# Kernel optimization log

Hardware: AMD Instinct MI355X
Metric: run time of the kernel (lower is better)

## Reference

```python
import jax, jax.numpy as jnp
import numpy as np

EMBED_DIM = 1024
NUM_HEADS = 16
HEAD_DIM = EMBED_DIM // NUM_HEADS
NEG = -1000000000.0


def setup_inputs() -> dict:
    key = jax.random.key(0)
    ks = jax.random.split(key, 13)
    B, S, D = 4, 2048, EMBED_DIM
    scale = 1.0 / np.sqrt(D)
    inp = {
        "query": jax.random.normal(ks[0], (B, S, D), jnp.float32),
        "key": jax.random.normal(ks[1], (B, S, D), jnp.float32),
        "value": jax.random.normal(ks[2], (B, S, D), jnp.float32),
        "mask": jax.random.randint(ks[3], (B, 1, 1, S), 0, 2, jnp.int32),
        "Wq": jax.random.normal(ks[4], (D, D), jnp.float32) * scale,
        "bq": jnp.zeros((D,), jnp.float32),
        "Wk": jax.random.normal(ks[5], (D, D), jnp.float32) * scale,
        "bk": jnp.zeros((D,), jnp.float32),
        "Wv": jax.random.normal(ks[6], (D, D), jnp.float32) * scale,
        "bv": jnp.zeros((D,), jnp.float32),
        "Wo": jax.random.normal(ks[7], (D, D), jnp.float32) * scale,
        "bo": jnp.zeros((D,), jnp.float32),
    }
    return inp


def _split_heads(x):
    B, S, D = x.shape
    return x.reshape(B, S, NUM_HEADS, HEAD_DIM).transpose(0, 2, 1, 3)  # [B,H,S,hd]


def reference(query, key, value, mask, Wq, bq, Wk, bk, Wv, bv, Wo, bo):
    B, S, D = query.shape
    Q = _split_heads(query @ Wq + bq)
    K = _split_heads(key @ Wk + bk)
    V = _split_heads(value @ Wv + bv)
    scores = jnp.einsum("bhqd,bhkd->bhqk", Q, K) / jnp.sqrt(jnp.float32(HEAD_DIM))
    scores = jnp.where(mask == 0, jnp.float32(NEG), scores)
    attn = jax.nn.softmax(scores, axis=-1)
    out = jnp.einsum("bhqk,bhkd->bhqd", attn, V)
    out = out.transpose(0, 2, 1, 3).reshape(B, S, D)
    return out @ Wo + bo
```

## Files before the change

kernel.cpp:

```cpp
#include <hip/hip_runtime.h>


#define SEQ   2048
#define EDIM  1024
#define NHEAD 16
#define HDIM  64
#define NBAT  4
#define MTOK  8192

typedef __attribute__((ext_vector_type(8))) __bf16 bf16x8;
typedef __attribute__((ext_vector_type(4))) __bf16 bf16x4;
typedef __attribute__((ext_vector_type(4))) float f32x4;
typedef __attribute__((ext_vector_type(16))) float f32x16;
typedef __attribute__((ext_vector_type(8))) unsigned short us8;
typedef unsigned short u16;

#define SCL   0.1803368801111244f

__device__ __forceinline__ u16 bfbits(float f) {
    __bf16 h = (__bf16)f;
    return __builtin_bit_cast(u16, h);
}
__device__ __forceinline__ bf16x8 bc(us8 v) { return __builtin_bit_cast(bf16x8, v); }
__device__ __forceinline__ float exp2fast(float x) {
    float r;
    asm("v_exp_f32 %0, %1" : "=v"(r) : "v"(x));
    return r;
}
__device__ __forceinline__ void glds16(const void* g, void* l) {
    __builtin_amdgcn_global_load_lds(
        (const __attribute__((address_space(1))) unsigned int*)g,
        (__attribute__((address_space(3))) unsigned int*)l, 16, 0, 0);
}

__global__ __launch_bounds__(256) void prep_kernel(const int* __restrict__ mask,
                                                   int* __restrict__ idxl,
                                                   int* __restrict__ cntp) {
    __shared__ int psum[257];
    const int b = blockIdx.x, t = threadIdx.x;
    const int* mp = mask + b * SEQ;
    int m8[8]; int s = 0;
#pragma unroll
    for (int i = 0; i < 8; ++i) { m8[i] = mp[t * 8 + i]; s += (m8[i] != 0); }
    psum[t + 1] = s;
    __syncthreads();
    if (t == 0) { psum[0] = 0; for (int i = 1; i <= 256; ++i) psum[i] += psum[i - 1]; }
    __syncthreads();
    int ex = psum[t];
#pragma unroll
    for (int i = 0; i < 8; ++i)
        if (m8[i] != 0) idxl[b * SEQ + (ex++)] = t * 8 + i;
    if (t == 0) cntp[b] = psum[256];
}

__global__ __launch_bounds__(256) void wtrans4_kernel(const float* __restrict__ W0,
                                                      const float* __restrict__ W1,
                                                      const float* __restrict__ W2,
                                                      const float* __restrict__ W3,
                                                      u16* __restrict__ WT) {
    __shared__ float tile[32][33];
    const int tx = threadIdx.x, ty = threadIdx.y;
    const int bx = blockIdx.x,  by = blockIdx.y, wz = blockIdx.z;
    const float* W = (wz == 0) ? W0 : (wz == 1) ? W1 : (wz == 2) ? W2 : W3;
    u16* O = WT + (size_t)wz * EDIM * EDIM;
#pragma unroll
    for (int i = 0; i < 4; ++i)
        tile[ty + i * 8][tx] = W[(size_t)(by * 32 + ty + i * 8) * EDIM + bx * 32 + tx];
    __syncthreads();
#pragma unroll
    for (int i = 0; i < 4; ++i) {
        int n = bx * 32 + ty + i * 8;
        int k = by * 32 + tx;
        O[(size_t)n * EDIM + k] = bfbits(tile[tx][ty + i * 8]);
    }
}

__global__ __launch_bounds__(256) void qkv_gemm_kernel(
        const float* __restrict__ Aq, const float* __restrict__ Ak,
        const float* __restrict__ Av, const u16* __restrict__ WTall,
        const float* __restrict__ bqp, const float* __restrict__ bkp,
        const float* __restrict__ bvp,
        u16* __restrict__ Qb, u16* __restrict__ Kb, u16* __restrict__ Vb,
        const int* __restrict__ idxl, const int* __restrict__ cntp) {
    const int id    = blockIdx.x;
    const int which = id >> 9;
    const int sub   = id & 511;
    const int r_    = sub >> 3;
    const int grp   = r_ >> 5, bnq = (r_ >> 2) & 7, bmin = r_ & 3;
    const int bm    = (sub & 7) + 8 * (grp * 4 + bmin);
    const int bn    = bnq;

    const float* A    = (which == 0) ? Aq : (which == 1) ? Ak : Av;
    const u16*   WT   = WTall + (size_t)which * EDIM * EDIM;
    const float* bias = (which == 0) ? bqp : (which == 1) ? bkp : bvp;
    u16*         outp = (which == 0) ? Qb : (which == 1) ? Kb : Vb;
    const float  oscale = (which == 1) ? SCL : 1.0f;
    const bool   gather = (which > 0);

    int cn = SEQ;
    if (gather) {
        cn = cntp[bm >> 4];
        if (((bm & 15) * 128) >= cn) return;
    }

    __shared__ __align__(16) float As[2][128 * 32];
    __shared__ __align__(16) u16   Bs[2][128][32];

    const int tid  = threadIdx.x;
    const int lane = tid & 63, w = tid >> 6;
    const int g    = lane >> 4, l15 = lane & 15;
    const int wrow = w >> 1, wcol = w & 1;

    const char* pa[4];
#pragma unroll
    for (int t = 0; t < 4; ++t) {
        const int rloc = w * 32 + t * 8 + (lane >> 3);
        int arow;
        if (gather) {
            const int sloc = (bm & 15) * 128 + rloc;
            const int gi = (sloc < cn) ? idxl[(bm >> 4) * SEQ + sloc] : 0;
            arow = (bm >> 4) * SEQ + gi;
        } else arow = bm * 128 + rloc;
        const int scol = ((lane & 7) ^ (lane >> 3)) * 4;
        pa[t] = (const char*)(A + (size_t)arow * EDIM + scol);
    }
    const char* pb[2];
#pragma unroll
    for (int t = 0; t < 2; ++t) {
        const int rloc = w * 32 + t * 16 + (lane >> 2);
        const int brow = bn * 128 + rloc;
        const int scol = ((lane & 3) ^ ((lane >> 3) & 3)) * 8;
        pb[t] = (const char*)(WT + (size_t)brow * EDIM + scol);
    }

    auto STAGE = [&](int bufn, int ko) {
        char* abase = (char*)&As[bufn][0] + w * 4096;
#pragma unroll
        for (int t = 0; t < 4; ++t)
            glds16(pa[t] + (size_t)ko * 4, abase + t * 1024);
        char* bbase = (char*)&Bs[bufn][0][0] + w * 2048;
#pragma unroll
        for (int t = 0; t < 2; ++t)
            glds16(pb[t] + (size_t)ko * 2, bbase + t * 1024);
    };

    f32x4 acc[4][4] = {};
    constexpr int NT = EDIM / 32;

    STAGE(0, 0);
    __syncthreads();

    int buf = 0;
#pragma unroll 1
    for (int kt = 0; kt < NT; ++kt) {
        if (kt < NT - 1) STAGE(buf ^ 1, (kt + 1) * 32);

        bf16x8 af[4], bfr[4];
        {
            const float* Ab = &As[buf][0];
            const int x = l15 & 7;
#pragma unroll
            for (int i = 0; i < 4; ++i) {
                const int row = wrow * 64 + i * 16 + l15;
                f32x4 u0 = *(const f32x4*)(Ab + row * 32 + (((2 * g)     ^ x) * 4));
                f32x4 u1 = *(const f32x4*)(Ab + row * 32 + (((2 * g + 1) ^ x) * 4));
#pragma unroll
                for (int j = 0; j < 4; ++j) {
                    af[i][j]     = (__bf16)u0[j];
                    af[i][4 + j] = (__bf16)u1[j];
                }
            }
        }
        {
            const int x = (l15 >> 1) & 3;
#pragma unroll
            for (int j = 0; j < 4; ++j) {
                const int row = wcol * 64 + j * 16 + l15;
                bfr[j] = bc(*(const us8*)((const u16*)&Bs[buf][0][0] + row * 32 + ((g ^ x) * 8)));
            }
        }

#pragma unroll
        for (int i = 0; i < 4; ++i)
#pragma unroll
            for (int j = 0; j < 4; ++j)
                acc[i][j] = __builtin_amdgcn_mfma_f32_16x16x32_bf16(af[i], bfr[j], acc[i][j], 0, 0, 0);

        __syncthreads();
        buf ^= 1;
    }

#pragma unroll
    for (int i = 0; i < 4; ++i) {
#pragma unroll
        for (int j = 0; j < 4; ++j) {
            const int gm0 = bm * 128 + wrow * 64 + i * 16 + g * 4;
            const int gn  = bn * 128 + wcol * 64 + j * 16 + l15;
            const float bv = bias[gn];
#pragma unroll
            for (int r = 0; r < 4; ++r) {
                float val = (acc[i][j][r] + bv) * oscale;
                const int m = gm0 + r;
                if (gather && (m & 2047) >= cn) val = 0.f;
                const int b = m >> 11, s = m & 2047;
                const int h = gn >> 6, d = gn & 63;
                if (which == 2)
                    outp[((size_t)(b * NHEAD + h) << 17) + d * SEQ + s] = bfbits(val);
                else
                    outp[((size_t)(b * NHEAD + h) << 17) + s * HDIM + d] = bfbits(val);
            }
        }
    }
}

__global__ __launch_bounds__(256) void o_gemm_kernel(const u16* __restrict__ Ap,
                                                     const u16* __restrict__ WT,
                                                     const float* __restrict__ bias,
                                                     float* __restrict__ outp) {
    const int id  = blockIdx.x;
    const int r_  = id >> 3;
    const int grp = r_ >> 5, bnq = (r_ >> 2) & 7, bmin = r_ & 3;
    const int bm  = (id & 7) + 8 * (grp * 4 + bmin);
    const int bn  = bnq;

    __shared__ __align__(16) u16 As[2][128][32];
    __shared__ __align__(16) u16 Bs[2][128][32];

    const int tid  = threadIdx.x;
    const int lane = tid & 63, w = tid >> 6;
    const int g    = lane >> 4, l15 = lane & 15;
    const int wrow = w >> 1, wcol = w & 1;

    const char* pa[2]; const char* pb[2];
#pragma unroll
    for (int t = 0; t < 2; ++t) {
        const int rloc = w * 32 + t * 16 + (lane >> 2);
        const int scol = ((lane & 3) ^ ((lane >> 3) & 3)) * 8;
        pa[t] = (const char*)(Ap + (size_t)(bm * 128 + rloc) * EDIM + scol);
        pb[t] = (const char*)(WT + (size_t)(bn * 128 + rloc) * EDIM + scol);
    }

    auto STAGE = [&](int bufn, int ko) {
        char* abase = (char*)&As[bufn][0][0] + w * 2048;
        char* bbase = (char*)&Bs[bufn][0][0] + w * 2048;
#pragma unroll
        for (int t = 0; t < 2; ++t) {
            glds16(pa[t] + (size_t)ko * 2, abase + t * 1024);
            glds16(pb[t] + (size_t)ko * 2, bbase + t * 1024);
        }
    };

    f32x4 acc[4][4] = {};
    constexpr int NT = EDIM / 32;

    STAGE(0, 0);
    __syncthreads();

    int buf = 0;
#pragma unroll 1
    for (int kt = 0; kt < NT; ++kt) {
        if (kt < NT - 1) STAGE(buf ^ 1, (kt + 1) * 32);

        bf16x8 af[4], bfr[4];
        const int x = (l15 >> 1) & 3;
#pragma unroll
        for (int i = 0; i < 4; ++i) {
            const int rowA = wrow * 64 + i * 16 + l15;
            af[i] = bc(*(const us8*)((const u16*)&As[buf][0][0] + rowA * 32 + ((g ^ x) * 8)));
            const int rowB = wcol * 64 + i * 16 + l15;
            bfr[i] = bc(*(const us8*)((const u16*)&Bs[buf][0][0] + rowB * 32 + ((g ^ x) * 8)));
        }

#pragma unroll
        for (int i = 0; i < 4; ++i)
#pragma unroll
            for (int j = 0; j < 4; ++j)
                acc[i][j] = __builtin_amdgcn_mfma_f32_16x16x32_bf16(af[i], bfr[j], acc[i][j], 0, 0, 0);

        __syncthreads();
        buf ^= 1;
    }

#pragma unroll
    for (int i = 0; i < 4; ++i) {
#pragma unroll
        for (int j = 0; j < 4; ++j) {
            const int gm0 = bm * 128 + wrow * 64 + i * 16 + g * 4;
            const int gn  = bn * 128 + wcol * 64 + j * 16 + l15;
            const float bv = bias[gn];
#pragma unroll
            for (int r = 0; r < 4; ++r)
                outp[(size_t)(gm0 + r) * EDIM + gn] = acc[i][j][r] + bv;
        }
    }
}

__global__ __launch_bounds__(256) void attn_kernel(const u16* __restrict__ Q,
                                                   const u16* __restrict__ K,
                                                   const u16* __restrict__ VT,
                                                   const int* __restrict__ cntp,
                                                   u16* __restrict__ O) {
    __shared__ u16 Klds[2][64][64];
    __shared__ u16 Vlds[2][64][64];

    const int tid = threadIdx.x, lane = tid & 63, w = tid >> 6;
    const int h = lane >> 5, l31 = lane & 31;

    const int id  = blockIdx.x;
    const int bh  = (id & 7) * 8 + ((id >> 3) >> 4);
    const int qb  = (id >> 3) & 15;
    const int b   = bh >> 4, hd_ = bh & 15;

    const u16* Qp = Q + ((size_t)bh << 17);
    const u16* Kp = K + ((size_t)bh << 17);
    const u16* Vp = VT + ((size_t)bh << 17);
    const int q0w = qb * 128 + w * 32;

    const int cn  = cntp[b];
    const int ktc = (cn + 63) >> 6;

    bf16x8 qf[4];
#pragma unroll
    for (int khd = 0; khd < 4; ++khd)
        qf[khd] = bc(*(const us8*)&Qp[(size_t)(q0w + l31) * HDIM + khd * 16 + h * 8]);

    const int b_  = l31 & 3, hp = (l31 >> 2) & 1, cc = l31 >> 3;
    const int piR = 16 * (cc & 1) + 8 * hp + 4 * (cc >> 1) + b_;
    const int swk = b_ | (hp << 2);
    const int swv = l31 & 7;

    const int lr = lane >> 3, lg = lane & 7;
    const u16* pKs[2]; const u16* pVs[2];
#pragma unroll
    for (int t = 0; t < 2; ++t) {
        const int rloc = w * 16 + t * 8 + lr;
        const int xk = (rloc & 3) | (((rloc >> 3) & 1) << 2);
        pKs[t] = Kp + (size_t)rloc * HDIM + ((lg ^ xk) << 3);
        const int xv = rloc & 7;
        pVs[t] = Vp + (size_t)rloc * SEQ + ((lg ^ xv) << 3);
    }

    auto STAGE = [&](int bufn, int kb) {
#pragma unroll
        for (int t = 0; t < 2; ++t) {
            glds16(pKs[t] + (size_t)kb * HDIM, &Klds[bufn][w * 16 + t * 8][0]);
            glds16(pVs[t] + kb,                &Vlds[bufn][w * 16 + t * 8][0]);
        }
    };

    f32x16 ot[2] = {};
    f32x16 ls = {};

    bf16x8 onesf;
#pragma unroll
    for (int j = 0; j < 8; ++j) onesf[j] = (__bf16)1.0f;

    STAGE(0, 0);
    __syncthreads();

    for (int kt = 0; kt < ktc; ++kt) {
        const int cur = kt & 1;
        const bool more = (kt + 1) < ktc;
        if (more) STAGE(cur ^ 1, (kt + 1) * 64);

        f32x16 st[2] = {};
        __builtin_amdgcn_s_setprio(1);
#pragma unroll
        for (int kb2 = 0; kb2 < 2; ++kb2) {
            const u16* Kr = &Klds[cur][kb2 * 32 + piR][0];
#pragma unroll
            for (int khd = 0; khd < 4; ++khd) {
                bf16x8 kf = bc(*(const us8*)&Kr[(khd * 16 + h * 8) ^ (swk << 3)]);
                st[kb2] = __builtin_amdgcn_mfma_f32_32x32x16_bf16(kf, qf[khd], st[kb2], 0, 0, 0);
            }
        }
        __builtin_amdgcn_s_setprio(0);

#pragma unroll
        for (int kb2 = 0; kb2 < 2; ++kb2)
#pragma unroll
            for (int e = 0; e < 16; ++e)
                st[kb2][e] = exp2fast(st[kb2][e]);

        if (kt == ktc - 1) {
            const int kbase = kt * 64;
#pragma unroll
            for (int kb2 = 0; kb2 < 2; ++kb2)
#pragma unroll
                for (int cp = 0; cp < 4; ++cp)
#pragma unroll
                    for (int j = 0; j < 4; ++j) {
                        const int key = kbase + kb2 * 32 + 16 * (cp & 1) + 4 * (cp >> 1) + 8 * h + j;
                        if (key >= cn) st[kb2][cp * 4 + j] = 0.f;
                    }
        }

        bf16x8 pf[4];
#pragma unroll
        for (int s = 0; s < 4; ++s) {
            const int kb2 = s >> 1, sel = (s & 1) * 4;
#pragma unroll
            for (int j = 0; j < 4; ++j) {
                pf[s][j]     = (__bf16)st[kb2][sel + j];
                pf[s][4 + j] = (__bf16)st[kb2][8 + sel + j];
            }
        }

        __builtin_amdgcn_s_setprio(1);
#pragma unroll
        for (int s = 0; s < 4; ++s)
            ls = __builtin_amdgcn_mfma_f32_32x32x16_bf16(onesf, pf[s], ls, 0, 0, 0);
#pragma unroll
        for (int dblk = 0; dblk < 2; ++dblk) {
            const u16* Vr = &Vlds[cur][dblk * 32 + l31][0];
#pragma unroll
            for (int s = 0; s < 4; ++s) {
                bf16x8 vf = bc(*(const us8*)&Vr[(s * 16 + h * 8) ^ (swv << 3)]);
                ot[dblk] = __builtin_amdgcn_mfma_f32_32x32x16_bf16(vf, pf[s], ot[dblk], 0, 0, 0);
            }
        }
        __builtin_amdgcn_s_setprio(0);

        __syncthreads();
    }

    const float inv = 1.f / ls[0];

    const size_t row = (size_t)(b * SEQ + q0w + l31) * EDIM + hd_ * HDIM;
#pragma unroll
    for (int dblk = 0; dblk < 2; ++dblk) {
#pragma unroll
        for (int cp = 0; cp < 4; ++cp) {
            bf16x4 t;
#pragma unroll
            for (int j = 0; j < 4; ++j)
                t[j] = (__bf16)(ot[dblk][cp * 4 + j] * inv);
            *(bf16x4*)&O[row + dblk * 32 + 8 * cp + 4 * h] = t;
        }
    }
}

extern "C" void kernel_launch(void* const* d_in, const int* in_sizes, int n_in,
                              void* d_out, int out_size, void* d_ws, size_t ws_size,
                              hipStream_t stream) {
    const float* query = (const float*)d_in[0];
    const float* key   = (const float*)d_in[1];
    const float* value = (const float*)d_in[2];
    const int*   mask  = (const int*)d_in[3];
    const float* Wq = (const float*)d_in[4];  const float* bq = (const float*)d_in[5];
    const float* Wk = (const float*)d_in[6];  const float* bk = (const float*)d_in[7];
    const float* Wv = (const float*)d_in[8];  const float* bv = (const float*)d_in[9];
    const float* Wo = (const float*)d_in[10]; const float* bo = (const float*)d_in[11];

    char* ws = (char*)d_ws;
    const size_t WT_BYTES  = (size_t)EDIM * EDIM * 2;
    const size_t BUF_BYTES = (size_t)MTOK * EDIM * 2;
    u16* wtq   = (u16*)(ws);
    u16* wto   = (u16*)(ws + 3 * WT_BYTES);
    u16* Qbuf  = (u16*)(ws + 4 * WT_BYTES);
    u16* Kbuf  = (u16*)(ws + 4 * WT_BYTES + BUF_BYTES);
    u16* VTbuf = (u16*)(ws + 4 * WT_BYTES + 2 * BUF_BYTES);
    u16* Abuf  = (u16*)(ws + 4 * WT_BYTES + 3 * BUF_BYTES);
    int* idxl  = (int*)(ws + 4 * WT_BYTES + 4 * BUF_BYTES);
    int* cntp  = (int*)(ws + 4 * WT_BYTES + 4 * BUF_BYTES + (size_t)MTOK * 4);

    prep_kernel<<<NBAT, 256, 0, stream>>>(mask, idxl, cntp);

    dim3 tgrid(32, 32, 4), tblk(32, 8);
    wtrans4_kernel<<<tgrid, tblk, 0, stream>>>(Wq, Wk, Wv, Wo, wtq);

    qkv_gemm_kernel<<<1536, 256, 0, stream>>>(query, key, value, wtq,
                                              bq, bk, bv, Qbuf, Kbuf, VTbuf,
                                              idxl, cntp);

    attn_kernel<<<1024, 256, 0, stream>>>(Qbuf, Kbuf, VTbuf, cntp, Abuf);

    o_gemm_kernel<<<512, 256, 0, stream>>>(Abuf, wto, bo, (float*)d_out);
}
```

Baseline: 179.7 us.

## Convert A tile to bf16 in registers before LDS store in QKV GEMM

The fp32 activation tile for the QKV projection GEMM is now loaded into registers, converted to bf16 once, and written to LDS as bf16, replacing async global-to-LDS copies of fp32 data. Each element is now converted once per block rather than once per consuming wave, and the A tile takes half the LDS space and read bandwidth. The price is that the A global load is no longer a direct LDS copy: its latency must be hidden by the MFMA work between the register load and the deferred LDS write, and register pressure goes up.

```diff
diff --git a/kernel.cpp b/kernel.cpp
--- a/kernel.cpp
+++ b/kernel.cpp
@@ -103,27 +103,30 @@
         if (((bm & 15) * 128) >= cn) return;
     }
 
-    __shared__ __align__(16) float As[2][128 * 32];
-    __shared__ __align__(16) u16   Bs[2][128][32];
+    __shared__ __align__(16) u16 As[2][128][32];
+    __shared__ __align__(16) u16 Bs[2][128][32];
 
     const int tid  = threadIdx.x;
     const int lane = tid & 63, w = tid >> 6;
     const int g    = lane >> 4, l15 = lane & 15;
     const int wrow = w >> 1, wcol = w & 1;
 
-    const char* pa[4];
-#pragma unroll
-    for (int t = 0; t < 4; ++t) {
-        const int rloc = w * 32 + t * 8 + (lane >> 3);
+    const float* paf[2];
+    int rlocA[2];
+#pragma unroll
+    for (int t = 0; t < 2; ++t) {
+        const int rloc = w * 32 + t * 16 + (lane >> 2);
+        rlocA[t] = rloc;
         int arow;
         if (gather) {
             const int sloc = (bm & 15) * 128 + rloc;
             const int gi = (sloc < cn) ? idxl[(bm >> 4) * SEQ + sloc] : 0;
             arow = (bm >> 4) * SEQ + gi;
         } else arow = bm * 128 + rloc;
-        const int scol = ((lane & 7) ^ (lane >> 3)) * 4;
-        pa[t] = (const char*)(A + (size_t)arow * EDIM + scol);
-    }
+        paf[t] = A + (size_t)arow * EDIM + (lane & 3) * 8;
+    }
+    const int xA = ((lane & 3) ^ ((lane >> 3) & 3)) * 8;
+
     const char* pb[2];
 #pragma unroll
     for (int t = 0; t < 2; ++t) {
@@ -133,11 +136,27 @@
         pb[t] = (const char*)(WT + (size_t)brow * EDIM + scol);
     }
 
-    auto STAGE = [&](int bufn, int ko) {
-        char* abase = (char*)&As[bufn][0] + w * 4096;
-#pragma unroll
-        for (int t = 0; t < 4; ++t)
-            glds16(pa[t] + (size_t)ko * 4, abase + t * 1024);
+    f32x4 ar[2][2];
+    auto LOAD_A = [&](int ko) {
+#pragma unroll
+        for (int t = 0; t < 2; ++t) {
+            ar[t][0] = *(const f32x4*)(paf[t] + ko);
+            ar[t][1] = *(const f32x4*)(paf[t] + ko + 4);
+        }
+    };
+    auto WRITE_A = [&](int bufn) {
+#pragma unroll
+        for (int t = 0; t < 2; ++t) {
+            bf16x8 o;
+#pragma unroll
+            for (int j = 0; j < 4; ++j) {
+                o[j]     = (__bf16)ar[t][0][j];
+                o[4 + j] = (__bf16)ar[t][1][j];
+            }
+            *(bf16x8*)&As[bufn][rlocA[t]][xA] = o;
+        }
+    };
+    auto STAGE_B = [&](int bufn, int ko) {
         char* bbase = (char*)&Bs[bufn][0][0] + w * 2048;
 #pragma unroll
         for (int t = 0; t < 2; ++t)
@@ -147,37 +166,28 @@
     f32x4 acc[4][4] = {};
     constexpr int NT = EDIM / 32;
 
-    STAGE(0, 0);
+    LOAD_A(0);
+    STAGE_B(0, 0);
+    WRITE_A(0);
     __syncthreads();
 
     int buf = 0;
 #pragma unroll 1
     for (int kt = 0; kt < NT; ++kt) {
-        if (kt < NT - 1) STAGE(buf ^ 1, (kt + 1) * 32);
+        const bool more = kt + 1 < NT;
+        if (more) {
+            LOAD_A((kt + 1) * 32);
+            STAGE_B(buf ^ 1, (kt + 1) * 32);
+        }
 
         bf16x8 af[4], bfr[4];
-        {
-            const float* Ab = &As[buf][0];
-            const int x = l15 & 7;
-#pragma unroll
-            for (int i = 0; i < 4; ++i) {
-                const int row = wrow * 64 + i * 16 + l15;
-                f32x4 u0 = *(const f32x4*)(Ab + row * 32 + (((2 * g)     ^ x) * 4));
-                f32x4 u1 = *(const f32x4*)(Ab + row * 32 + (((2 * g + 1) ^ x) * 4));
-#pragma unroll
-                for (int j = 0; j < 4; ++j) {
-                    af[i][j]     = (__bf16)u0[j];
-                    af[i][4 + j] = (__bf16)u1[j];
-                }
-            }
-        }
-        {
-            const int x = (l15 >> 1) & 3;
-#pragma unroll
-            for (int j = 0; j < 4; ++j) {
-                const int row = wcol * 64 + j * 16 + l15;
-                bfr[j] = bc(*(const us8*)((const u16*)&Bs[buf][0][0] + row * 32 + ((g ^ x) * 8)));
-            }
+        const int x = (l15 >> 1) & 3;
+#pragma unroll
+        for (int i = 0; i < 4; ++i) {
+            const int rowA = wrow * 64 + i * 16 + l15;
+            af[i] = bc(*(const us8*)((const u16*)&As[buf][0][0] + rowA * 32 + ((g ^ x) * 8)));
+            const int rowB = wcol * 64 + i * 16 + l15;
+            bfr[i] = bc(*(const us8*)((const u16*)&Bs[buf][0][0] + rowB * 32 + ((g ^ x) * 8)));
         }
 
 #pragma unroll
@@ -186,6 +196,7 @@
             for (int j = 0; j < 4; ++j)
                 acc[i][j] = __builtin_amdgcn_mfma_f32_16x16x32_bf16(af[i], bfr[j], acc[i][j], 0, 0, 0);
 
+        if (more) WRITE_A(buf ^ 1);
         __syncthreads();
         buf ^= 1;
     }
```

After: 192.1 us. 6.9% more time.

## Pre-convert and gather Q/K/V inputs to bf16 before the QKV GEMM

Applied to the files above, without the earlier changes.

Adds a separate kernel that casts the fp32 query/key/value activations to bf16 and compacts the unmasked key/value rows into contiguous buffers, zero-padding up to the next 128-row tile. The QKV GEMM then streams bf16 A tiles with the same swizzled LDS layout as the weights, which halves its A-side LDS footprint and global traffic and drops the per-fragment fp32-to-bf16 conversion and row-index gather. In exchange, an extra pass reads all fp32 inputs once and writes bf16 copies, and the new buffers share workspace with the attention output buffer.

```diff
diff --git a/kernel.cpp b/kernel.cpp
--- a/kernel.cpp
+++ b/kernel.cpp
@@ -75,13 +75,59 @@
     }
 }
 
+__global__ __launch_bounds__(256) void cvtg_kernel(const float* __restrict__ q,
+                                                   const float* __restrict__ k,
+                                                   const float* __restrict__ v,
+                                                   const int* __restrict__ idxl,
+                                                   const int* __restrict__ cntp,
+                                                   u16* __restrict__ oq,
+                                                   u16* __restrict__ ok,
+                                                   u16* __restrict__ ov) {
+    const int sel  = blockIdx.y;
+    const int grow = blockIdx.x * 4 + (threadIdx.x >> 6);
+    const int col  = (threadIdx.x & 63) * 16;
+    const float* src;
+    u16* dst;
+    if (sel == 0) {
+        src = q + (size_t)grow * EDIM;
+        dst = oq + (size_t)grow * EDIM;
+    } else {
+        const int b = grow >> 11, j = grow & 2047;
+        const int cn = cntp[b];
+        dst = (sel == 1 ? ok : ov) + (size_t)grow * EDIM;
+        if (j < cn) {
+            const int gi = idxl[b * SEQ + j];
+            src = (sel == 1 ? k : v) + ((size_t)(b * SEQ + gi)) * EDIM;
+        } else {
+            if (j < ((cn + 127) & ~127)) {
+                us8 z = {};
+                *(us8*)(dst + col) = z;
+                *(us8*)(dst + col + 8) = z;
+            }
+            return;
+        }
+    }
+    f32x4 v0 = *(const f32x4*)(src + col);
+    f32x4 v1 = *(const f32x4*)(src + col + 4);
+    f32x4 v2 = *(const f32x4*)(src + col + 8);
+    f32x4 v3 = *(const f32x4*)(src + col + 12);
+    us8 r0, r1;
+#pragma unroll
+    for (int j2 = 0; j2 < 4; ++j2) {
+        r0[j2] = bfbits(v0[j2]); r0[4 + j2] = bfbits(v1[j2]);
+        r1[j2] = bfbits(v2[j2]); r1[4 + j2] = bfbits(v3[j2]);
+    }
+    *(us8*)(dst + col) = r0;
+    *(us8*)(dst + col + 8) = r1;
+}
+
 __global__ __launch_bounds__(256) void qkv_gemm_kernel(
-        const float* __restrict__ Aq, const float* __restrict__ Ak,
-        const float* __restrict__ Av, const u16* __restrict__ WTall,
+        const u16* __restrict__ Aq, const u16* __restrict__ Ak,
+        const u16* __restrict__ Av, const u16* __restrict__ WTall,
         const float* __restrict__ bqp, const float* __restrict__ bkp,
         const float* __restrict__ bvp,
         u16* __restrict__ Qb, u16* __restrict__ Kb, u16* __restrict__ Vb,
-        const int* __restrict__ idxl, const int* __restrict__ cntp) {
+        const int* __restrict__ cntp) {
     const int id    = blockIdx.x;
     const int which = id >> 9;
     const int sub   = id & 511;
@@ -90,58 +136,43 @@
     const int bm    = (sub & 7) + 8 * (grp * 4 + bmin);
     const int bn    = bnq;
 
-    const float* A    = (which == 0) ? Aq : (which == 1) ? Ak : Av;
+    const u16*   A    = (which == 0) ? Aq : (which == 1) ? Ak : Av;
     const u16*   WT   = WTall + (size_t)which * EDIM * EDIM;
     const float* bias = (which == 0) ? bqp : (which == 1) ? bkp : bvp;
     u16*         outp = (which == 0) ? Qb : (which == 1) ? Kb : Vb;
     const float  oscale = (which == 1) ? SCL : 1.0f;
-    const bool   gather = (which > 0);
 
     int cn = SEQ;
-    if (gather) {
+    if (which > 0) {
         cn = cntp[bm >> 4];
         if (((bm & 15) * 128) >= cn) return;
     }
 
-    __shared__ __align__(16) float As[2][128 * 32];
-    __shared__ __align__(16) u16   Bs[2][128][32];
+    __shared__ __align__(16) u16 As[2][128][32];
+    __shared__ __align__(16) u16 Bs[2][128][32];
 
     const int tid  = threadIdx.x;
     const int lane = tid & 63, w = tid >> 6;
     const int g    = lane >> 4, l15 = lane & 15;
     const int wrow = w >> 1, wcol = w & 1;
 
-    const char* pa[4];
-#pragma unroll
-    for (int t = 0; t < 4; ++t) {
-        const int rloc = w * 32 + t * 8 + (lane >> 3);
-        int arow;
-        if (gather) {
-            const int sloc = (bm & 15) * 128 + rloc;
-            const int gi = (sloc < cn) ? idxl[(bm >> 4) * SEQ + sloc] : 0;
-            arow = (bm >> 4) * SEQ + gi;
-        } else arow = bm * 128 + rloc;
-        const int scol = ((lane & 7) ^ (lane >> 3)) * 4;
-        pa[t] = (const char*)(A + (size_t)arow * EDIM + scol);
-    }
-    const char* pb[2];
+    const char* pa[2]; const char* pb[2];
 #pragma unroll
     for (int t = 0; t < 2; ++t) {
         const int rloc = w * 32 + t * 16 + (lane >> 2);
-        const int brow = bn * 128 + rloc;
         const int scol = ((lane & 3) ^ ((lane >> 3) & 3)) * 8;
-        pb[t] = (const char*)(WT + (size_t)brow * EDIM + scol);
+        pa[t] = (const char*)(A + (size_t)(bm * 128 + rloc) * EDIM + scol);
+        pb[t] = (const char*)(WT + (size_t)(bn * 128 + rloc) * EDIM + scol);
     }
 
     auto STAGE = [&](int bufn, int ko) {
-        char* abase = (char*)&As[bufn][0] + w * 4096;
-#pragma unroll
-        for (int t = 0; t < 4; ++t)
-            glds16(pa[t] + (size_t)ko * 4, abase + t * 1024);
+        char* abase = (char*)&As[bufn][0][0] + w * 2048;
         char* bbase = (char*)&Bs[bufn][0][0] + w * 2048;
 #pragma unroll
-        for (int t = 0; t < 2; ++t)
+        for (int t = 0; t < 2; ++t) {
+            glds16(pa[t] + (size_t)ko * 2, abase + t * 1024);
             glds16(pb[t] + (size_t)ko * 2, bbase + t * 1024);
+        }
     };
 
     f32x4 acc[4][4] = {};
@@ -156,28 +187,13 @@
         if (kt < NT - 1) STAGE(buf ^ 1, (kt + 1) * 32);
 
         bf16x8 af[4], bfr[4];
-        {
-            const float* Ab = &As[buf][0];
-            const int x = l15 & 7;
-#pragma unroll
-            for (int i = 0; i < 4; ++i) {
-                const int row = wrow * 64 + i * 16 + l15;
-                f32x4 u0 = *(const f32x4*)(Ab + row * 32 + (((2 * g)     ^ x) * 4));
-                f32x4 u1 = *(const f32x4*)(Ab + row * 32 + (((2 * g + 1) ^ x) * 4));
-#pragma unroll
-                for (int j = 0; j < 4; ++j) {
-                    af[i][j]     = (__bf16)u0[j];
-                    af[i][4 + j] = (__bf16)u1[j];
-                }
-            }
-        }
-        {
-            const int x = (l15 >> 1) & 3;
-#pragma unroll
-            for (int j = 0; j < 4; ++j) {
-                const int row = wcol * 64 + j * 16 + l15;
-                bfr[j] = bc(*(const us8*)((const u16*)&Bs[buf][0][0] + row * 32 + ((g ^ x) * 8)));
-            }
+        const int x = (l15 >> 1) & 3;
+#pragma unroll
+        for (int i = 0; i < 4; ++i) {
+            const int rowA = wrow * 64 + i * 16 + l15;
+            af[i] = bc(*(const us8*)((const u16*)&As[buf][0][0] + rowA * 32 + ((g ^ x) * 8)));
+            const int rowB = wcol * 64 + i * 16 + l15;
+            bfr[i] = bc(*(const us8*)((const u16*)&Bs[buf][0][0] + rowB * 32 + ((g ^ x) * 8)));
         }
 
 #pragma unroll
@@ -201,7 +217,7 @@
             for (int r = 0; r < 4; ++r) {
                 float val = (acc[i][j][r] + bv) * oscale;
                 const int m = gm0 + r;
-                if (gather && (m & 2047) >= cn) val = 0.f;
+                if (which > 0 && (m & 2047) >= cn) val = 0.f;
                 const int b = m >> 11, s = m & 2047;
                 const int h = gn >> 6, d = gn & 63;
                 if (which == 2)
@@ -460,18 +476,25 @@
     u16* Qbuf  = (u16*)(ws + 4 * WT_BYTES);
     u16* Kbuf  = (u16*)(ws + 4 * WT_BYTES + BUF_BYTES);
     u16* VTbuf = (u16*)(ws + 4 * WT_BYTES + 2 * BUF_BYTES);
-    u16* Abuf  = (u16*)(ws + 4 * WT_BYTES + 3 * BUF_BYTES);
-    int* idxl  = (int*)(ws + 4 * WT_BYTES + 4 * BUF_BYTES);
-    int* cntp  = (int*)(ws + 4 * WT_BYTES + 4 * BUF_BYTES + (size_t)MTOK * 4);
+    char* X    = ws + 4 * WT_BYTES + 3 * BUF_BYTES;
+    u16* Qbf   = (u16*)X;
+    u16* Kc    = (u16*)(X + BUF_BYTES);
+    u16* Vc    = (u16*)(X + 2 * BUF_BYTES);
+    u16* Abuf  = (u16*)X;
+    int* idxl  = (int*)(X + 3 * BUF_BYTES);
+    int* cntp  = (int*)(X + 3 * BUF_BYTES + (size_t)MTOK * 4);
 
     prep_kernel<<<NBAT, 256, 0, stream>>>(mask, idxl, cntp);
 
     dim3 tgrid(32, 32, 4), tblk(32, 8);
     wtrans4_kernel<<<tgrid, tblk, 0, stream>>>(Wq, Wk, Wv, Wo, wtq);
 
-    qkv_gemm_kernel<<<1536, 256, 0, stream>>>(query, key, value, wtq,
+    cvtg_kernel<<<dim3(2048, 3), 256, 0, stream>>>(query, key, value,
+                                                   idxl, cntp, Qbf, Kc, Vc);
+
+    qkv_gemm_kernel<<<1536, 256, 0, stream>>>(Qbf, Kc, Vc, wtq,
                                               bq, bk, bv, Qbuf, Kbuf, VTbuf,
-                                              idxl, cntp);
+                                              cntp);
 
     attn_kernel<<<1024, 256, 0, stream>>>(Qbuf, Kbuf, VTbuf, cntp, Abuf);
 
```

Result: no change. 182.7 us (+1.7%).
